# Optimization experiments

Hardware: AMD Instinct MI355X
Metric: run time of the kernel (lower is better)

## Reference

```python
import jax, jax.numpy as jnp
import numpy as np

IN_CH = 128
N_HEAD = 16
D_K = 4
D_MODEL = 256
T_PE = 1000.0
EPS = 1e-5


def setup_inputs() -> dict:
    key = jax.random.key(0)
    ks = jax.random.split(key, 8)
    sz_b, L, h, w = 4, 30, 64, 64
    x = jax.random.normal(ks[0], (sz_b, L, IN_CH, h, w), dtype=jnp.float32)
    batch_positions = jnp.sort(jax.random.randint(ks[1], (sz_b, L), 0, 365), axis=1).astype(jnp.int32)
    pad_mask = jnp.zeros((sz_b, L), dtype=bool)
    gn_weight = jnp.ones((IN_CH,), dtype=jnp.float32)
    gn_bias = jnp.zeros((IN_CH,), dtype=jnp.float32)
    conv_w = jax.random.normal(ks[2], (D_MODEL, IN_CH), dtype=jnp.float32) * (1.0 / np.sqrt(IN_CH))
    conv_b = jnp.zeros((D_MODEL,), dtype=jnp.float32)
    Q = jax.random.normal(ks[3], (N_HEAD, D_K), dtype=jnp.float32) * np.sqrt(2.0 / D_K)
    Wk = jax.random.normal(ks[4], (N_HEAD * D_K, D_MODEL), dtype=jnp.float32) * np.sqrt(2.0 / D_K)
    bk = jnp.zeros((N_HEAD * D_K,), dtype=jnp.float32)
    return {"x": x, "gn_weight": gn_weight, "gn_bias": gn_bias,
            "conv_w": conv_w, "conv_b": conv_b, "Q": Q, "Wk": Wk, "bk": bk,
            "batch_positions": batch_positions, "pad_mask": pad_mask}


def reference(x, gn_weight, gn_bias, conv_w, conv_b, Q, Wk, bk, batch_positions, pad_mask):
    n_head, d_k = Q.shape
    sz_b, L, d, h, w = x.shape
    B = sz_b * h * w
    # flatten pixels: [B, L, C]
    out = x.transpose(0, 3, 4, 1, 2).reshape(B, L, d)
    # GroupNorm(num_groups=n_head) over channels and time per pixel-sample
    g = out.transpose(0, 2, 1).reshape(B, n_head, d // n_head, L)
    mu = g.mean(axis=(2, 3), keepdims=True)
    var = g.var(axis=(2, 3), keepdims=True)
    g = (g - mu) / jnp.sqrt(var + EPS)
    out = g.reshape(B, d, L) * gn_weight[None, :, None] + gn_bias[None, :, None]
    out = out.transpose(0, 2, 1)  # [B, L, C]
    # 1x1 Conv1d == per-timestep linear projection to d_model
    out = out @ conv_w.T + conv_b  # [B, L, d_model]
    d_model = conv_w.shape[0]
    # sinusoidal positional encoding on dates, repeated over heads
    d_pe = d_model // n_head
    idx = jnp.arange(d_pe)
    denom = jnp.power(jnp.float32(T_PE), 2.0 * (idx // 2).astype(jnp.float32) / d_pe)
    tab = batch_positions.astype(jnp.float32)[:, :, None] / denom  # [sz_b, L, d_pe]
    pe = jnp.where(idx % 2 == 0, jnp.sin(tab), jnp.cos(tab))
    pe = jnp.tile(pe, (1, 1, n_head))  # [sz_b, L, d_model]
    out = (out.reshape(sz_b, h * w, L, d_model) + pe[:, None, :, :]).reshape(B, L, d_model)
    # keys and learned-query attention scores, temperature = sqrt(d_k)
    k = (out @ Wk.T + bk).reshape(B, L, n_head, d_k)
    scores = jnp.einsum('hd,blhd->hbl', Q, k) / jnp.sqrt(jnp.float32(d_k))
    scores = scores.reshape(n_head, sz_b, h * w, L)
    scores = jnp.where(pad_mask[None, :, None, :], jnp.float32(-1000.0), scores)
    attn = jax.nn.softmax(scores, axis=-1)
    # [n_head, sz_b, L, h, w]
    return attn.reshape(n_head, sz_b, h, w, L).transpose(0, 1, 4, 2, 3)
```

## Files before the change

kernel.cpp:

```cpp
#include <hip/hip_runtime.h>


#define EPSV 1e-5f

#define WS_U    0
#define WS_UU   2048
#define WS_P2   2304
#define WS_FLAG 4224
#define WS_QT   4352
#define WS_WT   8448
#define WS_INV  10496
#define WS_MUI  272640

__global__ void __launch_bounds__(256) k01(const float* __restrict__ Q,
                                           const float* __restrict__ Wk,
                                           const float* __restrict__ conv_w,
                                           const float* __restrict__ gn_w,
                                           const float* __restrict__ conv_b,
                                           const float* __restrict__ gn_b,
                                           const float* __restrict__ bk,
                                           const int* __restrict__ bpos,
                                           const unsigned char* __restrict__ pmask,
                                           const float* __restrict__ x,
                                           float* __restrict__ ws) {
    __shared__ float sc[16];
    __shared__ float qsv[256];
    __shared__ float rden[16];
    int t = threadIdx.x;
    int bx = blockIdx.x;
    if (bx == 512) {
        for (int i = t; i < 4096; i += 256) {
            int h = i >> 8, m = i & 255;
            float s = 0.f;
            #pragma unroll
            for (int d = 0; d < 4; ++d) s += Q[h*4+d] * Wk[(h*4+d)*256 + m];
            ws[WS_QT + h*256 + m] = s;
        }
        __syncthreads();
        for (int i = t; i < 2048; i += 256) {
            int h = i >> 7, c = i & 127;
            const float* qt = ws + WS_QT + h*256;
            float s = 0.f;
            #pragma unroll 32
            for (int m = 0; m < 256; ++m) s += qt[m] * conv_w[m*128 + c];
            ws[WS_WT + h*128 + c] = s;
            ws[WS_U  + c*16  + h] = s * gn_w[c];
        }
        __syncthreads();
        {
            int h = t >> 4, g = t & 15;
            float s = 0.f;
            #pragma unroll
            for (int cc = 0; cc < 8; ++cc) s += ws[WS_U + (g*8+cc)*16 + h];
            ws[WS_UU + g*16 + h] = s;
            float q = 0.f;
            #pragma unroll
            for (int r = 0; r < 16; ++r) q += ws[WS_QT + h*256 + r*16 + g];
            qsv[h*16 + g] = q;
        }
        if (t < 16) {
            int h = t;
            float wb = 0.f;
            #pragma unroll 16
            for (int c = 0; c < 128; ++c) wb += ws[WS_WT + h*128 + c] * gn_b[c];
            float s0 = 0.f;
            #pragma unroll 16
            for (int m = 0; m < 256; ++m) s0 += ws[WS_QT + h*256 + m] * conv_b[m];
            #pragma unroll
            for (int d = 0; d < 4; ++d) s0 += Q[h*4+d] * bk[h*4+d];
            sc[h] = wb + s0;
            rden[t] = powf(1000.0f, -((float)(t >> 1)) * 0.125f);
        }
        if (t < 120) ws[WS_FLAG + t] = pmask[t] ? 1.f : 0.f;
        __syncthreads();
        for (int idx = t; idx < 1920; idx += 256) {
            int h = idx / 120, r = idx - h*120;
            float pos = (float)bpos[r];
            float pt = 0.f;
            #pragma unroll
            for (int p = 0; p < 16; ++p) {
                float tab = pos * rden[p];
                float v = (p & 1) ? cosf(tab) : sinf(tab);
                pt += v * qsv[h*16 + p];
            }
            ws[WS_P2 + r*16 + h] = pt + sc[h];
        }
        return;
    }
    int g = bx >> 5;
    int pq = (bx & 31)*256 + t;
    int pix0 = pq*2;
    int b = pix0 >> 12, pij = pix0 & 4095;
    const float2* xp = (const float2*)(x + (b*30*128 + g*8)*4096 + pij);
    float sx = 0.f, sy = 0.f, ssx = 0.f, ssy = 0.f;
    for (int l = 0; l < 30; ++l) {
        const float2* xl = xp + l*128*2048;
        #pragma unroll
        for (int c = 0; c < 8; ++c) {
            float2 v = xl[c*2048];
            sx += v.x; sy += v.y;
            ssx += v.x*v.x; ssy += v.y*v.y;
        }
    }
    float mux = sx*(1.f/240.f), muy = sy*(1.f/240.f);
    float ivx = rsqrtf(ssx*(1.f/240.f) - mux*mux + EPSV);
    float ivy = rsqrtf(ssy*(1.f/240.f) - muy*muy + EPSV);
    *(float2*)(ws + WS_INV + g*16384 + pix0) = make_float2(ivx, ivy);
    *(float2*)(ws + WS_MUI + g*16384 + pix0) = make_float2(mux*ivx, muy*ivy);
}

#define FMA4(A, S, V) { (A).x += (S)*(V).x; (A).y += (S)*(V).y; (A).z += (S)*(V).z; (A).w += (S)*(V).w; }
#define NMA4(A, S, V) { (A).x -= (S)*(V).x; (A).y -= (S)*(V).y; (A).z -= (S)*(V).z; (A).w -= (S)*(V).w; }

__global__ void __launch_bounds__(256) k2(const float* __restrict__ x,
                                          const float* __restrict__ ws,
                                          float* __restrict__ out) {
    __shared__ float su[2048];
    __shared__ float sU[256];
    __shared__ float sP2[16];
    __shared__ float sflag;
    int t = threadIdx.x;
    int bx = blockIdx.x;
    int pb2 = bx / 30, l = bx - pb2*30;
    int pixbase = pb2 * 1024;
    int b = pixbase >> 12;
    int pijb = pixbase & 4095;
    int bl = b*30 + l;
    int pij = pijb + t*4;
    int pix0 = pixbase + t*4;

    for (int i = t; i < 512; i += 256)
        *(float4*)(su + i*4) = *(const float4*)(ws + WS_U + i*4);
    sU[t] = ws[WS_UU + t];
    if (t < 16) sP2[t] = ws[WS_P2 + bl*16 + t];
    if (t == 0) sflag = ws[WS_FLAG + bl];
    __syncthreads();

    float4 acc[16];
    #pragma unroll
    for (int h = 0; h < 16; ++h) acc[h] = make_float4(0.f, 0.f, 0.f, 0.f);
    const float* xbase = x + (bl*128)*4096 + pij;
    #pragma unroll 2
    for (int g = 0; g < 16; ++g) {
        float4 inv = *(const float4*)(ws + WS_INV + g*16384 + pix0);
        float4 mui = *(const float4*)(ws + WS_MUI + g*16384 + pix0);
        const float* us = su + g*128;
        #pragma unroll
        for (int q = 0; q < 4; ++q) {
            float4 Ug = *(const float4*)(sU + g*16 + q*4);
            NMA4(acc[q*4+0], Ug.x, mui); NMA4(acc[q*4+1], Ug.y, mui);
            NMA4(acc[q*4+2], Ug.z, mui); NMA4(acc[q*4+3], Ug.w, mui);
        }
        const float* xg = xbase + g*8*4096;
        #pragma unroll
        for (int cc = 0; cc < 8; ++cc) {
            float4 v = *(const float4*)(xg + cc*4096);
            float4 xs;
            xs.x = v.x*inv.x; xs.y = v.y*inv.y; xs.z = v.z*inv.z; xs.w = v.w*inv.w;
            #pragma unroll
            for (int q = 0; q < 4; ++q) {
                float4 uq = *(const float4*)(us + cc*16 + q*4);
                FMA4(acc[q*4+0], uq.x, xs); FMA4(acc[q*4+1], uq.y, xs);
                FMA4(acc[q*4+2], uq.z, xs); FMA4(acc[q*4+3], uq.w, xs);
            }
        }
    }
    bool msk = (sflag != 0.f);
    #pragma unroll
    for (int h = 0; h < 16; ++h) {
        float p2 = sP2[h];
        float4 sv;
        sv.x = 0.5f*(acc[h].x + p2); sv.y = 0.5f*(acc[h].y + p2);
        sv.z = 0.5f*(acc[h].z + p2); sv.w = 0.5f*(acc[h].w + p2);
        if (msk) sv = make_float4(-1000.f, -1000.f, -1000.f, -1000.f);
        *(float4*)(out + ((h*4 + b)*30 + l)*4096 + pij) = sv;
    }
}

__global__ void __launch_bounds__(256) k3(float* __restrict__ out) {
    int idx = blockIdx.x*256 + threadIdx.x;
    int hb = idx >> 11;
    int pij = (idx & 2047)*2;
    float* p = out + hb*30*4096 + pij;
    float2 v[30];
    float m0 = -1e30f, m1 = -1e30f;
    #pragma unroll
    for (int l = 0; l < 30; ++l) {
        v[l] = *(const float2*)(p + l*4096);
        m0 = fmaxf(m0, v[l].x); m1 = fmaxf(m1, v[l].y);
    }
    float s0 = 0.f, s1 = 0.f;
    #pragma unroll
    for (int l = 0; l < 30; ++l) {
        v[l].x = __expf(v[l].x - m0); s0 += v[l].x;
        v[l].y = __expf(v[l].y - m1); s1 += v[l].y;
    }
    float r0 = 1.f/s0, r1 = 1.f/s1;
    #pragma unroll
    for (int l = 0; l < 30; ++l) {
        *(float2*)(p + l*4096) = make_float2(v[l].x*r0, v[l].y*r1);
    }
}

extern "C" void kernel_launch(void* const* d_in, const int* in_sizes, int n_in,
                              void* d_out, int out_size, void* d_ws, size_t ws_size,
                              hipStream_t stream) {
    const float* x      = (const float*)d_in[0];
    const float* gn_w   = (const float*)d_in[1];
    const float* gn_b   = (const float*)d_in[2];
    const float* conv_w = (const float*)d_in[3];
    const float* conv_b = (const float*)d_in[4];
    const float* Q      = (const float*)d_in[5];
    const float* Wk     = (const float*)d_in[6];
    const float* bk     = (const float*)d_in[7];
    const int*   bpos   = (const int*)d_in[8];
    const unsigned char* pmask = (const unsigned char*)d_in[9];
    float* ws  = (float*)d_ws;
    float* out = (float*)d_out;

    hipLaunchKernelGGL(k01, dim3(513), dim3(256), 0, stream,
                       Q, Wk, conv_w, gn_w, conv_b, gn_b, bk, bpos, pmask, x, ws);
    hipLaunchKernelGGL(k2,  dim3(480), dim3(256), 0, stream, x, ws, out);
    hipLaunchKernelGGL(k3,  dim3(512), dim3(256), 0, stream, out);
}
```

Baseline: 165.5 us.

## Split GroupNorm statistics pass over time chunks with partial-sum reduction kernel

The stats pass previously used 512 blocks, each looping over all 30 timesteps. It now uses 960 blocks, each covering two timesteps with float4 loads. Partial sums and sums of squares go to the output buffer as scratch, and a new reduce kernel combines them into inv/mu*inv. The parameter-precompute block also parallelises its bias dot products with shared-memory reductions. This adds a kernel launch and extra scratch traffic in exchange for more parallelism and latency hiding on the large read of x.

```diff
diff --git a/kernel.cpp b/kernel.cpp
--- a/kernel.cpp
+++ b/kernel.cpp
@@ -12,23 +12,28 @@
 #define WS_INV  10496
 #define WS_MUI  272640
 
-__global__ void __launch_bounds__(256) k01(const float* __restrict__ Q,
-                                           const float* __restrict__ Wk,
-                                           const float* __restrict__ conv_w,
-                                           const float* __restrict__ gn_w,
-                                           const float* __restrict__ conv_b,
-                                           const float* __restrict__ gn_b,
-                                           const float* __restrict__ bk,
-                                           const int* __restrict__ bpos,
-                                           const unsigned char* __restrict__ pmask,
-                                           const float* __restrict__ x,
-                                           float* __restrict__ ws) {
-    __shared__ float sc[16];
-    __shared__ float qsv[256];
-    __shared__ float rden[16];
+#define PS_OFF(g,b,lc) (((((g)*4+(b))*15)+(lc))*4096)
+#define PSS_BASE 3932160
+
+__global__ void __launch_bounds__(256) k1(const float* __restrict__ Q,
+                                          const float* __restrict__ Wk,
+                                          const float* __restrict__ conv_w,
+                                          const float* __restrict__ gn_w,
+                                          const float* __restrict__ conv_b,
+                                          const float* __restrict__ gn_b,
+                                          const float* __restrict__ bk,
+                                          const int* __restrict__ bpos,
+                                          const unsigned char* __restrict__ pmask,
+                                          const float* __restrict__ x,
+                                          float* __restrict__ ws,
+                                          float* __restrict__ pscratch) {
     int t = threadIdx.x;
     int bx = blockIdx.x;
-    if (bx == 512) {
+    if (bx >= 960) {
+        __shared__ float red[256];
+        __shared__ float sc[16];
+        __shared__ float qsv[256];
+        __shared__ float rden[16];
         for (int i = t; i < 4096; i += 256) {
             int h = i >> 8, m = i & 255;
             float s = 0.f;
@@ -48,27 +53,44 @@
         }
         __syncthreads();
         {
-            int h = t >> 4, g = t & 15;
-            float s = 0.f;
-            #pragma unroll
-            for (int cc = 0; cc < 8; ++cc) s += ws[WS_U + (g*8+cc)*16 + h];
-            ws[WS_UU + g*16 + h] = s;
+            int h = t >> 4, g2 = t & 15;
+            float s = 0.f;
+            #pragma unroll
+            for (int cc = 0; cc < 8; ++cc) s += ws[WS_U + (g2*8+cc)*16 + h];
+            ws[WS_UU + g2*16 + h] = s;
             float q = 0.f;
             #pragma unroll
-            for (int r = 0; r < 16; ++r) q += ws[WS_QT + h*256 + r*16 + g];
-            qsv[h*16 + g] = q;
-        }
+            for (int r = 0; r < 16; ++r) q += ws[WS_QT + h*256 + r*16 + g2];
+            qsv[h*16 + g2] = q;
+        }
+        {
+            int h = t >> 4, p = t & 15;
+            float s = 0.f;
+            #pragma unroll
+            for (int i = 0; i < 8; ++i) { int c = p*8+i; s += ws[WS_WT + h*128 + c] * gn_b[c]; }
+            red[t] = s;
+        }
+        __syncthreads();
+        if (t < 16) { float wb = 0.f;
+            #pragma unroll
+            for (int p = 0; p < 16; ++p) wb += red[t*16+p];
+            sc[t] = wb; }
+        __syncthreads();
+        {
+            int h = t >> 4, p = t & 15;
+            float s = 0.f;
+            #pragma unroll
+            for (int i = 0; i < 16; ++i) { int m = p*16+i; s += ws[WS_QT + h*256 + m] * conv_b[m]; }
+            red[t] = s;
+        }
+        __syncthreads();
         if (t < 16) {
-            int h = t;
-            float wb = 0.f;
-            #pragma unroll 16
-            for (int c = 0; c < 128; ++c) wb += ws[WS_WT + h*128 + c] * gn_b[c];
             float s0 = 0.f;
-            #pragma unroll 16
-            for (int m = 0; m < 256; ++m) s0 += ws[WS_QT + h*256 + m] * conv_b[m];
-            #pragma unroll
-            for (int d = 0; d < 4; ++d) s0 += Q[h*4+d] * bk[h*4+d];
-            sc[h] = wb + s0;
+            #pragma unroll
+            for (int p = 0; p < 16; ++p) s0 += red[t*16+p];
+            #pragma unroll
+            for (int d = 0; d < 4; ++d) s0 += Q[t*4+d] * bk[t*4+d];
+            sc[t] += s0;
             rden[t] = powf(1000.0f, -((float)(t >> 1)) * 0.125f);
         }
         if (t < 120) ws[WS_FLAG + t] = pmask[t] ? 1.f : 0.f;
@@ -87,26 +109,60 @@
         }
         return;
     }
-    int g = bx >> 5;
-    int pq = (bx & 31)*256 + t;
-    int pix0 = pq*2;
-    int b = pix0 >> 12, pij = pix0 & 4095;
-    const float2* xp = (const float2*)(x + (b*30*128 + g*8)*4096 + pij);
-    float sx = 0.f, sy = 0.f, ssx = 0.f, ssy = 0.f;
-    for (int l = 0; l < 30; ++l) {
-        const float2* xl = xp + l*128*2048;
-        #pragma unroll
+    int b  = bx / 240;
+    int rem = bx - b*240;
+    int lc = rem >> 4;
+    int g  = rem & 15;
+    const float* xb = x + (((b*30 + lc*2)*128) + g*8)*4096 + t*4;
+    float4 s0 = make_float4(0.f,0.f,0.f,0.f), s1 = s0, s2 = s0, s3 = s0;
+    float4 q0 = s0, q1 = s0, q2 = s0, q3 = s0;
+    #pragma unroll
+    for (int l = 0; l < 2; ++l) {
+        const float* xl = xb + l*128*4096;
+        #pragma unroll 2
         for (int c = 0; c < 8; ++c) {
-            float2 v = xl[c*2048];
-            sx += v.x; sy += v.y;
-            ssx += v.x*v.x; ssy += v.y*v.y;
-        }
-    }
-    float mux = sx*(1.f/240.f), muy = sy*(1.f/240.f);
-    float ivx = rsqrtf(ssx*(1.f/240.f) - mux*mux + EPSV);
-    float ivy = rsqrtf(ssy*(1.f/240.f) - muy*muy + EPSV);
-    *(float2*)(ws + WS_INV + g*16384 + pix0) = make_float2(ivx, ivy);
-    *(float2*)(ws + WS_MUI + g*16384 + pix0) = make_float2(mux*ivx, muy*ivy);
+            const float* xc = xl + c*4096;
+            float4 v0 = *(const float4*)(xc);
+            float4 v1 = *(const float4*)(xc + 1024);
+            float4 v2 = *(const float4*)(xc + 2048);
+            float4 v3 = *(const float4*)(xc + 3072);
+            s0.x += v0.x; s0.y += v0.y; s0.z += v0.z; s0.w += v0.w;
+            q0.x += v0.x*v0.x; q0.y += v0.y*v0.y; q0.z += v0.z*v0.z; q0.w += v0.w*v0.w;
+            s1.x += v1.x; s1.y += v1.y; s1.z += v1.z; s1.w += v1.w;
+            q1.x += v1.x*v1.x; q1.y += v1.y*v1.y; q1.z += v1.z*v1.z; q1.w += v1.w*v1.w;
+            s2.x += v2.x; s2.y += v2.y; s2.z += v2.z; s2.w += v2.w;
+            q2.x += v2.x*v2.x; q2.y += v2.y*v2.y; q2.z += v2.z*v2.z; q2.w += v2.w*v2.w;
+            s3.x += v3.x; s3.y += v3.y; s3.z += v3.z; s3.w += v3.w;
+            q3.x += v3.x*v3.x; q3.y += v3.y*v3.y; q3.z += v3.z*v3.z; q3.w += v3.w*v3.w;
+        }
+    }
+    float* ps  = pscratch + PS_OFF(g,b,lc) + t*4;
+    float* pss = ps + PSS_BASE;
+    *(float4*)(ps)        = s0;  *(float4*)(ps + 1024)  = s1;
+    *(float4*)(ps + 2048) = s2;  *(float4*)(ps + 3072)  = s3;
+    *(float4*)(pss)        = q0; *(float4*)(pss + 1024) = q1;
+    *(float4*)(pss + 2048) = q2; *(float4*)(pss + 3072) = q3;
+}
+
+__global__ void __launch_bounds__(256) k1r(const float* __restrict__ pscratch,
+                                           float* __restrict__ ws) {
+    int idx = blockIdx.x*256 + threadIdx.x;
+    int g = idx >> 14;
+    int pix = idx & 16383;
+    int b = pix >> 12, pij = pix & 4095;
+    const float* ps  = pscratch + PS_OFF(g,b,0) + pij;
+    const float* pss = ps + PSS_BASE;
+    float S = 0.f, SS = 0.f;
+    #pragma unroll
+    for (int lc = 0; lc < 15; ++lc) {
+        S  += ps[lc*4096];
+        SS += pss[lc*4096];
+    }
+    float mu  = S * (1.f/240.f);
+    float var = SS * (1.f/240.f) - mu*mu;
+    float inv = rsqrtf(var + EPSV);
+    ws[WS_INV + g*16384 + pix] = inv;
+    ws[WS_MUI + g*16384 + pix] = mu * inv;
 }
 
 #define FMA4(A, S, V) { (A).x += (S)*(V).x; (A).y += (S)*(V).y; (A).z += (S)*(V).z; (A).w += (S)*(V).w; }
@@ -218,8 +274,9 @@
     float* ws  = (float*)d_ws;
     float* out = (float*)d_out;
 
-    hipLaunchKernelGGL(k01, dim3(513), dim3(256), 0, stream,
-                       Q, Wk, conv_w, gn_w, conv_b, gn_b, bk, bpos, pmask, x, ws);
-    hipLaunchKernelGGL(k2,  dim3(480), dim3(256), 0, stream, x, ws, out);
-    hipLaunchKernelGGL(k3,  dim3(512), dim3(256), 0, stream, out);
-}
+    hipLaunchKernelGGL(k1,  dim3(961),  dim3(256), 0, stream,
+                       Q, Wk, conv_w, gn_w, conv_b, gn_b, bk, bpos, pmask, x, ws, out);
+    hipLaunchKernelGGL(k1r, dim3(1024), dim3(256), 0, stream, out, ws);
+    hipLaunchKernelGGL(k2,  dim3(480),  dim3(256), 0, stream, x, ws, out);
+    hipLaunchKernelGGL(k3,  dim3(512),  dim3(256), 0, stream, out);
+}
```

Measured after the change: 158.0 us. -4.5%, faster.

## Split GroupNorm stats into per-timestep partial sums plus a reduction kernel

Applied to the files above, without the earlier changes.

The stats kernel now runs 480 blocks, each reading one timestep slab of x with float4 loads, the same access pattern k2 uses. It writes per-timestep partial sums and sums of squares into the workspace. A new small kernel reduces them over the 30 timesteps into the inverse std and mean*inv. The serial per-head reductions in the setup block are also parallelised with shared-memory trees. This adds an extra launch and about 60 MB of partial-sum traffic, in exchange for better coalescing and parallelism in the first pass over x.

```diff
diff --git a/kernel.cpp b/kernel.cpp
--- a/kernel.cpp
+++ b/kernel.cpp
@@ -11,8 +11,15 @@
 #define WS_WT   8448
 #define WS_INV  10496
 #define WS_MUI  272640
-
-__global__ void __launch_bounds__(256) k01(const float* __restrict__ Q,
+#define PSF  1048576
+#define PSQ  8912896
+
+#define ACC4(S, Q, V) { (S).x += (V).x; (S).y += (V).y; (S).z += (V).z; (S).w += (V).w; \
+                        (Q).x += (V).x*(V).x; (Q).y += (V).y*(V).y; (Q).z += (V).z*(V).z; (Q).w += (V).w*(V).w; }
+#define FMA4(A, S, V) { (A).x += (S)*(V).x; (A).y += (S)*(V).y; (A).z += (S)*(V).z; (A).w += (S)*(V).w; }
+#define NMA4(A, S, V) { (A).x -= (S)*(V).x; (A).y -= (S)*(V).y; (A).z -= (S)*(V).z; (A).w -= (S)*(V).w; }
+
+__global__ void __launch_bounds__(256) k1a(const float* __restrict__ Q,
                                            const float* __restrict__ Wk,
                                            const float* __restrict__ conv_w,
                                            const float* __restrict__ gn_w,
@@ -23,12 +30,13 @@
                                            const unsigned char* __restrict__ pmask,
                                            const float* __restrict__ x,
                                            float* __restrict__ ws) {
-    __shared__ float sc[16];
-    __shared__ float qsv[256];
-    __shared__ float rden[16];
     int t = threadIdx.x;
     int bx = blockIdx.x;
-    if (bx == 512) {
+    if (bx >= 480) {
+        __shared__ float red[256];
+        __shared__ float sc[16];
+        __shared__ float qsv[256];
+        __shared__ float rden[16];
         for (int i = t; i < 4096; i += 256) {
             int h = i >> 8, m = i & 255;
             float s = 0.f;
@@ -48,27 +56,46 @@
         }
         __syncthreads();
         {
-            int h = t >> 4, g = t & 15;
-            float s = 0.f;
-            #pragma unroll
-            for (int cc = 0; cc < 8; ++cc) s += ws[WS_U + (g*8+cc)*16 + h];
-            ws[WS_UU + g*16 + h] = s;
+            int h = t >> 4, g2 = t & 15;
+            float s = 0.f;
+            #pragma unroll
+            for (int cc = 0; cc < 8; ++cc) s += ws[WS_U + (g2*8+cc)*16 + h];
+            ws[WS_UU + g2*16 + h] = s;
             float q = 0.f;
             #pragma unroll
-            for (int r = 0; r < 16; ++r) q += ws[WS_QT + h*256 + r*16 + g];
-            qsv[h*16 + g] = q;
-        }
+            for (int r = 0; r < 16; ++r) q += ws[WS_QT + h*256 + r*16 + g2];
+            qsv[h*16 + g2] = q;
+        }
+        {
+            int h = t >> 4, p = t & 15;
+            float s = 0.f;
+            #pragma unroll
+            for (int i = 0; i < 8; ++i) { int c = p*8+i; s += ws[WS_WT + h*128 + c] * gn_b[c]; }
+            red[t] = s;
+        }
+        __syncthreads();
         if (t < 16) {
-            int h = t;
             float wb = 0.f;
-            #pragma unroll 16
-            for (int c = 0; c < 128; ++c) wb += ws[WS_WT + h*128 + c] * gn_b[c];
+            #pragma unroll
+            for (int p = 0; p < 16; ++p) wb += red[t*16+p];
+            sc[t] = wb;
+        }
+        __syncthreads();
+        {
+            int h = t >> 4, p = t & 15;
+            float s = 0.f;
+            #pragma unroll
+            for (int i = 0; i < 16; ++i) { int m = p*16+i; s += ws[WS_QT + h*256 + m] * conv_b[m]; }
+            red[t] = s;
+        }
+        __syncthreads();
+        if (t < 16) {
             float s0 = 0.f;
-            #pragma unroll 16
-            for (int m = 0; m < 256; ++m) s0 += ws[WS_QT + h*256 + m] * conv_b[m];
-            #pragma unroll
-            for (int d = 0; d < 4; ++d) s0 += Q[h*4+d] * bk[h*4+d];
-            sc[h] = wb + s0;
+            #pragma unroll
+            for (int p = 0; p < 16; ++p) s0 += red[t*16+p];
+            #pragma unroll
+            for (int d = 0; d < 4; ++d) s0 += Q[t*4+d] * bk[t*4+d];
+            sc[t] += s0;
             rden[t] = powf(1000.0f, -((float)(t >> 1)) * 0.125f);
         }
         if (t < 120) ws[WS_FLAG + t] = pmask[t] ? 1.f : 0.f;
@@ -87,30 +114,58 @@
         }
         return;
     }
-    int g = bx >> 5;
-    int pq = (bx & 31)*256 + t;
-    int pix0 = pq*2;
-    int b = pix0 >> 12, pij = pix0 & 4095;
-    const float2* xp = (const float2*)(x + (b*30*128 + g*8)*4096 + pij);
-    float sx = 0.f, sy = 0.f, ssx = 0.f, ssy = 0.f;
-    for (int l = 0; l < 30; ++l) {
-        const float2* xl = xp + l*128*2048;
+    int pb2 = bx / 30, l = bx - pb2*30;
+    int pixbase = pb2 * 1024;
+    int b = pixbase >> 12;
+    int pijb = pixbase & 4095;
+    int bl = b*30 + l;
+    int pij = pijb + t*4;
+    int pix0 = pixbase + t*4;
+    const float* xbase = x + (bl*128)*4096 + pij;
+    float* psb = ws + PSF + (l*16)*16384 + pix0;
+    #pragma unroll 2
+    for (int g = 0; g < 16; ++g) {
+        const float* xg = xbase + g*8*4096;
+        float4 s = make_float4(0.f,0.f,0.f,0.f);
+        float4 q = make_float4(0.f,0.f,0.f,0.f);
         #pragma unroll
-        for (int c = 0; c < 8; ++c) {
-            float2 v = xl[c*2048];
-            sx += v.x; sy += v.y;
-            ssx += v.x*v.x; ssy += v.y*v.y;
-        }
-    }
-    float mux = sx*(1.f/240.f), muy = sy*(1.f/240.f);
-    float ivx = rsqrtf(ssx*(1.f/240.f) - mux*mux + EPSV);
-    float ivy = rsqrtf(ssy*(1.f/240.f) - muy*muy + EPSV);
-    *(float2*)(ws + WS_INV + g*16384 + pix0) = make_float2(ivx, ivy);
-    *(float2*)(ws + WS_MUI + g*16384 + pix0) = make_float2(mux*ivx, muy*ivy);
-}
-
-#define FMA4(A, S, V) { (A).x += (S)*(V).x; (A).y += (S)*(V).y; (A).z += (S)*(V).z; (A).w += (S)*(V).w; }
-#define NMA4(A, S, V) { (A).x -= (S)*(V).x; (A).y -= (S)*(V).y; (A).z -= (S)*(V).z; (A).w -= (S)*(V).w; }
+        for (int cc = 0; cc < 8; ++cc) {
+            float4 v = *(const float4*)(xg + cc*4096);
+            ACC4(s, q, v);
+        }
+        *(float4*)(psb + g*16384)              = s;
+        *(float4*)(psb + g*16384 + (PSQ-PSF))  = q;
+    }
+}
+
+__global__ void __launch_bounds__(256) k1r(float* __restrict__ ws) {
+    int bx = blockIdx.x;
+    int g = bx >> 4, pw = bx & 15;
+    int pix = pw*1024 + threadIdx.x*4;
+    const float* ps = ws + PSF + g*16384 + pix;
+    float4 S = make_float4(0.f,0.f,0.f,0.f);
+    float4 SS = make_float4(0.f,0.f,0.f,0.f);
+    #pragma unroll 5
+    for (int l = 0; l < 30; ++l) {
+        float4 a = *(const float4*)(ps + l*16*16384);
+        float4 b = *(const float4*)(ps + l*16*16384 + (PSQ-PSF));
+        S.x += a.x; S.y += a.y; S.z += a.z; S.w += a.w;
+        SS.x += b.x; SS.y += b.y; SS.z += b.z; SS.w += b.w;
+    }
+    float4 inv, mui;
+    {
+        float mu = S.x*(1.f/240.f); float va = SS.x*(1.f/240.f) - mu*mu;
+        inv.x = rsqrtf(va + EPSV); mui.x = mu*inv.x;
+        mu = S.y*(1.f/240.f); va = SS.y*(1.f/240.f) - mu*mu;
+        inv.y = rsqrtf(va + EPSV); mui.y = mu*inv.y;
+        mu = S.z*(1.f/240.f); va = SS.z*(1.f/240.f) - mu*mu;
+        inv.z = rsqrtf(va + EPSV); mui.z = mu*inv.z;
+        mu = S.w*(1.f/240.f); va = SS.w*(1.f/240.f) - mu*mu;
+        inv.w = rsqrtf(va + EPSV); mui.w = mu*inv.w;
+    }
+    *(float4*)(ws + WS_INV + g*16384 + pix) = inv;
+    *(float4*)(ws + WS_MUI + g*16384 + pix) = mui;
+}
 
 __global__ void __launch_bounds__(256) k2(const float* __restrict__ x,
                                           const float* __restrict__ ws,
@@ -218,8 +273,9 @@
     float* ws  = (float*)d_ws;
     float* out = (float*)d_out;
 
-    hipLaunchKernelGGL(k01, dim3(513), dim3(256), 0, stream,
+    hipLaunchKernelGGL(k1a, dim3(481), dim3(256), 0, stream,
                        Q, Wk, conv_w, gn_w, conv_b, gn_b, bk, bpos, pmask, x, ws);
+    hipLaunchKernelGGL(k1r, dim3(256), dim3(256), 0, stream, ws);
     hipLaunchKernelGGL(k2,  dim3(480), dim3(256), 0, stream, x, ws, out);
     hipLaunchKernelGGL(k3,  dim3(512), dim3(256), 0, stream, out);
 }
```

Result: slower. 171.5 us (+3.6%).
